# Optimization experiments

Measured on AMD Instinct MI355X. Metric: run time of the kernel, lower is better.

Reference implementation:

```python
import jax, jax.numpy as jnp
import numpy as np

SOS, EOS = 0, 29
B, S, ENC = 64, 800, 512      # batch, encoder seq len, encoder feature dim
T, V = 250, 30                # decode timesteps (training: y.shape[1]), vocab
E, H, D, P = 512, 512, 256, 256  # embed, lstm1 hidden, lstm2 hidden(=decoder_output), attention projection


def setup_inputs() -> dict:
    key = jax.random.key(0)
    ks = jax.random.split(key, 12)
    sc = lambda k, shape, s=0.05: jax.random.normal(k, shape, jnp.float32) * s
    embed_W = sc(ks[0], (V, E), 0.1).at[EOS].set(0.0)  # padding_idx=EOS row zeroed
    return dict(
        encoder_outputs=jax.random.normal(ks[1], (B, S, ENC), jnp.float32),
        embed_W=embed_W,
        W_ih1=sc(ks[2], (E + P, 4 * H)), b_ih1=jnp.zeros((4 * H,), jnp.float32),
        W_hh1=sc(ks[3], (H, 4 * H)),     b_hh1=jnp.zeros((4 * H,), jnp.float32),
        W_ih2=sc(ks[4], (H, 4 * D)),     b_ih2=jnp.zeros((4 * D,), jnp.float32),
        W_hh2=sc(ks[5], (D, 4 * D)),     b_hh2=jnp.zeros((4 * D,), jnp.float32),
        Wk=sc(ks[6], (ENC, P)), bk=jnp.zeros((P,), jnp.float32),
        Wv=sc(ks[7], (ENC, P)), bv=jnp.zeros((P,), jnp.float32),
        Wq=sc(ks[8], (D, P)),   bq=jnp.zeros((P,), jnp.float32),
        char_b=jnp.zeros((V,), jnp.float32),
        encoder_lens=jax.random.randint(ks[9], (B,), S // 2, S + 1),
        y=jax.random.randint(ks[10], (B, T), 0, V),
    )


def _lstm_cell(x, h, c, W_ih, b_ih, W_hh, b_hh):
    gates = x @ W_ih + b_ih + h @ W_hh + b_hh
    i, f, g, o = jnp.split(gates, 4, axis=-1)  # torch LSTMCell gate order
    c_new = jax.nn.sigmoid(f) * c + jax.nn.sigmoid(i) * jnp.tanh(g)
    h_new = jax.nn.sigmoid(o) * jnp.tanh(c_new)
    return h_new, c_new


def reference(encoder_outputs, embed_W, W_ih1, b_ih1, W_hh1, b_hh1,
              W_ih2, b_ih2, W_hh2, b_hh2, Wk, bk, Wv, bv, Wq, bq,
              char_b, encoder_lens, y):
    # set_key_value_mask: project encoder outputs once
    key_proj = encoder_outputs @ Wk + bk        # [B,S,P]
    val_proj = encoder_outputs @ Wv + bv        # [B,S,P]
    mask = jnp.arange(S)[None, :] < encoder_lens[:, None]  # [B,S]
    scale = 1.0 / jnp.sqrt(jnp.asarray(P, jnp.float32))

    # teacher-forced input embeddings: t=0 -> SOS, t>0 -> label_embed[:, t-1]
    label_embed = embed_W[y]                    # [B,T,E]
    sos = jnp.broadcast_to(embed_W[SOS][None, None, :], (1, B, E))
    char_seq = jnp.concatenate([sos, jnp.swapaxes(label_embed[:, :-1, :], 0, 1)], axis=0)  # [T,B,E]

    init = (jnp.zeros((B, H), jnp.float32), jnp.zeros((B, H), jnp.float32),
            jnp.zeros((B, D), jnp.float32), jnp.zeros((B, D), jnp.float32),
            key_proj[:, 0, :])                  # initial context = key[:,0,:]

    def step(carry, char_embed):
        h1, c1, h2, c2, context = carry
        x = jnp.concatenate([char_embed, context], axis=1)          # [B,E+P]
        h1, c1 = _lstm_cell(x, h1, c1, W_ih1, b_ih1, W_hh1, b_hh1)
        h2, c2 = _lstm_cell(h1, h2, c2, W_ih2, b_ih2, W_hh2, b_hh2)
        q = h2 @ Wq + bq                                            # [B,P]
        scores = jnp.einsum('bsp,bp->bs', key_proj, q) * scale      # [B,S]
        scores = jnp.where(mask, scores, -1e9)
        aw = jax.nn.softmax(scores, axis=1)                         # [B,S]
        context = jnp.einsum('bs,bsp->bp', aw, val_proj)            # [B,P]
        out_emb = jnp.concatenate([h2, context], axis=1)            # [B,2D]
        logits = out_emb @ embed_W.T + char_b                       # tied weights, [B,V]
        return (h1, c1, h2, c2, context), (logits, aw[0])

    _, (logits_T, aw0_T) = jax.lax.scan(step, init, char_seq)
    predictions = jnp.swapaxes(logits_T, 0, 1)   # [B,T,V]
    attention_plot = aw0_T.T                      # [S,T] (matches torch.stack(dim=1))
    return predictions, attention_plot
```

## Files before the change

kernel.cpp:

```cpp
#include <hip/hip_runtime.h>

typedef float f32x4 __attribute__((ext_vector_type(4)));
typedef short s16x8 __attribute__((ext_vector_type(8)));

#define MINI(a,b) ((a)<(b)?(a):(b))
#define MAXI(a,b) ((a)>(b)?(a):(b))

static __device__ __forceinline__ float bf2f(unsigned short u){
  union { unsigned int i; float f; } x; x.i = ((unsigned int)u) << 16; return x.f;
}
static __device__ __forceinline__ unsigned short f2bf(float f){
  union { float f; unsigned int i; } x; x.f = f;
  return (unsigned short)((x.i + 0x7fffu + ((x.i >> 16) & 1u)) >> 16);
}
static __device__ __forceinline__ float sigm(float x){ return 1.f / (1.f + __expf(-x)); }
static __device__ __forceinline__ float tanhf_(float x){ return 1.f - 2.f / (1.f + __expf(2.f * x)); }

static __device__ __forceinline__ float ald1(const float* p){
  return __hip_atomic_load(p, __ATOMIC_RELAXED, __HIP_MEMORY_SCOPE_AGENT);
}
static __device__ __forceinline__ void ast1(float* p, float v){
  __hip_atomic_store(p, v, __ATOMIC_RELAXED, __HIP_MEMORY_SCOPE_AGENT);
}
static __device__ __forceinline__ float2 ald2(const float* p){
  unsigned long long u = __hip_atomic_load((const unsigned long long*)p,
                          __ATOMIC_RELAXED, __HIP_MEMORY_SCOPE_AGENT);
  union { unsigned long long u; float2 f; } c; c.u = u; return c.f;
}
static __device__ __forceinline__ void ast2(float* p, float a, float b){
  union { unsigned long long u; float f[2]; } c; c.f[0] = a; c.f[1] = b;
  __hip_atomic_store((unsigned long long*)p, c.u, __ATOMIC_RELAXED, __HIP_MEMORY_SCOPE_AGENT);
}
static __device__ __forceinline__ unsigned long long ald64(const void* p){
  return __hip_atomic_load((const unsigned long long*)p, __ATOMIC_RELAXED, __HIP_MEMORY_SCOPE_AGENT);
}
static __device__ __forceinline__ void ast32(unsigned short* p, unsigned int v){
  __hip_atomic_store((unsigned int*)p, v, __ATOMIC_RELAXED, __HIP_MEMORY_SCOPE_AGENT);
}
static __device__ __forceinline__ void aadd(float* p, float v){
  __hip_atomic_fetch_add(p, v, __ATOMIC_RELAXED, __HIP_MEMORY_SCOPE_AGENT);
}

__global__ void k_prepw(const float* Wk, const float* Wq, const float* Wv,
                        const float* bk, const float* bq, const float* bv,
                        unsigned short* Bm, float* bvec, float* wkb, float* cb0){
  const int k = blockIdx.x;
  const int t = threadIdx.x;
  const float scale = 0.0625f;
  float acc = 0.f;
  for (int p = 0; p < 256; p++) acc += Wk[k*256+p] * Wq[t*256+p];
  Bm[(size_t)k*512 + t]       = f2bf(acc * scale);
  Bm[(size_t)k*512 + 256 + t] = f2bf(Wv[k*256+t]);
  __shared__ float red[256];
  red[t] = Wk[k*256+t] * bq[t];
  __syncthreads();
  for (int o = 128; o > 0; o >>= 1){ if (t < o) red[t] += red[t+o]; __syncthreads(); }
  if (t == 0) wkb[k] = red[0] * scale;
  if (k == 0){
    float a2 = 0.f;
    for (int p = 0; p < 256; p++) a2 += bk[p] * Wq[t*256+p];
    bvec[t] = a2 * scale;
    bvec[256+t] = bv[t];
    __syncthreads();
    red[t] = bk[t] * bq[t];
    __syncthreads();
    for (int o = 128; o > 0; o >>= 1){ if (t < o) red[t] += red[t+o]; __syncthreads(); }
    if (t == 0) *cb0 = red[0] * scale;
  }
}

__global__ void k_keybias(const float* enc, const float* wkb, const float* cb0,
                          float* keybias){
  const int m = blockIdx.x*8 + (threadIdx.x >> 6);
  const int lane = threadIdx.x & 63;
  float p = 0.f;
  #pragma unroll
  for (int j = 0; j < 8; j++){ int k = lane + 64*j; p += enc[(size_t)m*512 + k] * wkb[k]; }
  #pragma unroll
  for (int o = 1; o < 64; o <<= 1) p += __shfl_xor(p, o, 64);
  if (lane == 0) keybias[m] = p + *cb0;
}

__global__ void k_init(const float* enc, const float* Wk, const float* bk,
                       float* ctx, float* la, unsigned short* h1bf,
                       unsigned short* h2bf, float* h2f, float* c1p, float* c2p,
                       unsigned int* ctr){
  const int b = blockIdx.x, t = threadIdx.x;
  float acc = bk[t];
  const float* er = enc + (size_t)b*800*512;
  for (int k = 0; k < 512; k++) acc += er[k] * Wk[(size_t)k*256 + t];
  ctx[b*256 + t] = acc;
  if (t == 0) la[b] = 1.f;
  const int id = b*256 + t;
  unsigned int* h1u = (unsigned int*)h1bf;
  h1u[id] = 0u; h1u[16384 + id] = 0u;
  unsigned int* h2u = (unsigned int*)h2bf;
  h2u[id] = 0u;
  h2f[id] = 0.f; h2f[16384 + id] = 0.f;
  c1p[id] = 0.f; c1p[16384 + id] = 0.f;
  c2p[id] = 0.f;
  if (b == 0){ for (int i = t; i < 1024; i += 256) ctr[i] = 0u; }
}

__global__ __launch_bounds__(256) void k_gemm(const float* enc, const unsigned short* Bm,
                                              const float* bvec,
                                              unsigned short* kT, unsigned short* vl){
  __shared__ unsigned short Al[64][40];
  __shared__ unsigned short Bl[64][40];
  const int tid = threadIdx.x, w = tid >> 6, lane = tid & 63;
  const int M0 = (blockIdx.x >> 3) * 64;
  const int N0 = (blockIdx.x & 7) * 64;
  f32x4 acc[4] = {};
  const int mrow = w*16 + (lane & 15);
  const int koff = (lane >> 4) * 8;
  for (int k0 = 0; k0 < 512; k0 += 32){
    #pragma unroll
    for (int it = 0; it < 2; it++){
      int row = (tid >> 3) + it*32, kq = (tid & 7) * 4;
      float4 v = *(const float4*)(enc + (size_t)(M0+row)*512 + k0 + kq);
      Al[row][kq+0] = f2bf(v.x); Al[row][kq+1] = f2bf(v.y);
      Al[row][kq+2] = f2bf(v.z); Al[row][kq+3] = f2bf(v.w);
    }
    #pragma unroll
    for (int i = 0; i < 8; i++){
      int flat = tid*8 + i, kk = flat >> 6, n = flat & 63;
      Bl[n][kk] = Bm[(size_t)(k0+kk)*512 + N0 + n];
    }
    __syncthreads();
    s16x8 a = *(const s16x8*)&Al[mrow][koff];
    #pragma unroll
    for (int i = 0; i < 4; i++){
      s16x8 bb = *(const s16x8*)&Bl[i*16 + (lane & 15)][koff];
      acc[i] = __builtin_amdgcn_mfma_f32_16x16x32_bf16(a, bb, acc[i], 0, 0, 0);
    }
    __syncthreads();
  }
  #pragma unroll
  for (int i = 0; i < 4; i++){
    int n = N0 + i*16 + (lane & 15);
    float bb = bvec[n];
    #pragma unroll
    for (int r = 0; r < 4; r++){
      int m = M0 + w*16 + (lane >> 4)*4 + r;
      int b = m / 800, s = m - b*800;
      unsigned short hv = f2bf(acc[i][r] + bb);
      if (n < 256) kT[(size_t)b*204800 + (size_t)n*800 + s] = hv;
      else         vl[(size_t)b*204800 + (size_t)s*256 + (n-256)] = hv;
    }
  }
}

static __device__ __forceinline__ void gbar(unsigned int* ctrs, unsigned int* gen){
  __syncthreads();
  if (threadIdx.x == 0){
    *gen += 256u;
    const unsigned int target = *gen;
    __hip_atomic_fetch_add(&ctrs[(blockIdx.x & 15) * 32], 1u,
                           __ATOMIC_RELAXED, __HIP_MEMORY_SCOPE_AGENT);
    if (blockIdx.x == 0){
      for (;;){
        unsigned int s = 0;
        #pragma unroll
        for (int i = 0; i < 16; i++)
          s += __hip_atomic_load(&ctrs[i * 32], __ATOMIC_RELAXED, __HIP_MEMORY_SCOPE_AGENT);
        if (s >= target) break;
        __builtin_amdgcn_s_sleep(2);
      }
      #pragma unroll
      for (int i = 0; i < 16; i++)
        __hip_atomic_store(&ctrs[512 + i*32], target, __ATOMIC_RELAXED, __HIP_MEMORY_SCOPE_AGENT);
    } else {
      unsigned int* fl = &ctrs[512 + (blockIdx.x & 15)*32];
      while (__hip_atomic_load(fl, __ATOMIC_RELAXED, __HIP_MEMORY_SCOPE_AGENT) < target)
        __builtin_amdgcn_s_sleep(4);
    }
  }
  __syncthreads();
}

static __device__ __forceinline__ void dot_bf16(const unsigned short* xg, int k0, int k1,
                                                const float (*W)[8], float* acc){
  const unsigned long long* p = (const unsigned long long*)xg;
  int k = k0;
  while (k + 32 <= k1){
    unsigned long long v[8];
    #pragma unroll
    for (int i = 0; i < 8; i++) v[i] = ald64(p + (k >> 2) + i);
    #pragma unroll
    for (int i = 0; i < 8; i++){
      float xv[4];
      xv[0] = bf2f((unsigned short)v[i]);
      xv[1] = bf2f((unsigned short)(v[i] >> 16));
      xv[2] = bf2f((unsigned short)(v[i] >> 32));
      xv[3] = bf2f((unsigned short)(v[i] >> 48));
      #pragma unroll
      for (int d = 0; d < 4; d++){
        const float* wr = W[k + i*4 + d];
        #pragma unroll
        for (int cc = 0; cc < 8; cc++) acc[cc] += xv[d] * wr[cc];
      }
    }
    k += 32;
  }
  if (k < k1){
    unsigned long long v[4];
    #pragma unroll
    for (int i = 0; i < 4; i++) v[i] = ald64(p + (k >> 2) + i);
    #pragma unroll
    for (int i = 0; i < 4; i++){
      float xv[4];
      xv[0] = bf2f((unsigned short)v[i]);
      xv[1] = bf2f((unsigned short)(v[i] >> 16));
      xv[2] = bf2f((unsigned short)(v[i] >> 32));
      xv[3] = bf2f((unsigned short)(v[i] >> 48));
      #pragma unroll
      for (int d = 0; d < 4; d++){
        const float* wr = W[k + i*4 + d];
        #pragma unroll
        for (int cc = 0; cc < 8; cc++) acc[cc] += xv[d] * wr[cc];
      }
    }
  }
}

static __device__ __forceinline__ void dot_f32(const float* xg, int k0, int k1,
                                               const float (*W)[8], float* acc){
  for (int k = k0; k < k1; k += 16){
    float2 v[8];
    #pragma unroll
    for (int i = 0; i < 8; i++) v[i] = ald2(xg + k + 2*i);
    #pragma unroll
    for (int i = 0; i < 8; i++){
      const float* w0 = W[k + 2*i];
      const float* w1 = W[k + 2*i + 1];
      #pragma unroll
      for (int cc = 0; cc < 8; cc++) acc[cc] += v[i].x*w0[cc] + v[i].y*w1[cc];
    }
  }
}

__global__ __launch_bounds__(1024) void k_decode(
    const float* W_ih1, const float* b_ih1, const float* W_hh1, const float* b_hh1,
    const float* W_ih2, const float* b_ih2, const float* W_hh2, const float* b_hh2,
    const float* embW, const float* char_b, const int* lens, const int* y,
    const unsigned short* kT, const unsigned short* vl, const float* keybias,
    unsigned short* h1bf, unsigned short* h2bf, float* h2f,
    float* ctxacc, float* lacc, float* c1p, float* c2p,
    float* esc, unsigned int* ctr, float* out)
{
  __shared__ float W1s[1280][8];
  __shared__ float W2s[768][8];
  __shared__ float b1s[8];
  __shared__ float b2s[8];
  __shared__ float embrow[512];
  __shared__ float chb;
  __shared__ float redA[16][8][64];
  __shared__ float g1s[8][64];
  __shared__ float partA[16][256];
  __shared__ float e_l[256];
  __shared__ float h2loc[256];

  const int bi = blockIdx.x;
  const int tid = threadIdx.x;
  const int w = tid >> 6;
  const int lane = tid & 63;

  for (int idx = tid; idx < 1280*8; idx += 1024){
    int k = idx >> 3, c = idx & 7;
    int col = ((c >> 1) << 9) + 2*bi + (c & 1);
    W1s[k][c] = (k < 768) ? W_ih1[(size_t)k*2048 + col] : W_hh1[(size_t)(k-768)*2048 + col];
  }
  if (bi < 128){
    for (int idx = tid; idx < 768*8; idx += 1024){
      int k = idx >> 3, c = idx & 7;
      int col = ((c >> 1) << 8) + 2*bi + (c & 1);
      W2s[k][c] = (k < 512) ? W_ih2[(size_t)k*1024 + col] : W_hh2[(size_t)(k-512)*1024 + col];
    }
    if (tid < 8){ int col = ((tid >> 1) << 8) + 2*bi + (tid & 1); b2s[tid] = b_ih2[col] + b_hh2[col]; }
  }
  if (tid < 8){ int col = ((tid >> 1) << 9) + 2*bi + (tid & 1); b1s[tid] = b_ih1[col] + b_hh1[col]; }
  if (bi >= 128 && bi < 158){
    if (tid < 512) embrow[tid] = embW[(bi-128)*512 + tid];
    if (tid == 0) chb = char_b[bi-128];
  }
  __syncthreads();

  unsigned int gen = 0;
  const int myb = bi & 63;
  const int sc  = bi >> 6;
  const int mylen = lens[myb];
  const int sbase = sc * 200;

  float* preds = out;
  float* plot  = out + 480000;

  for (int t = 0; t < 250; ++t){
    const int p  = t & 1;
    const int np = 1 - p;
    const unsigned short* h1p_bf = h1bf + p*(64*512);
    unsigned short*       h1n_bf = h1bf + np*(64*512);
    const unsigned short* h2p_bf = h2bf + p*(64*256);
    unsigned short*       h2n_bf = h2bf + np*(64*256);
    const float* h2f_p = h2f + p*(64*256);
    float*       h2f_np= h2f + np*(64*256);
    const float* ca_p  = ctxacc + p*(64*256);
    float*       ca_np = ctxacc + np*(64*256);
    const float* la_p  = lacc + p*64;
    float*       la_np = lacc + np*64;

    {
      float acc[8]  = {0,0,0,0,0,0,0,0};
      float accB[8] = {0,0,0,0,0,0,0,0};
      const int b = lane;
      const int tok = (t == 0) ? 0 : y[b*250 + (t-1)];
      const float* erow = embW + (size_t)tok*512;
      const float* crow = ca_p + b*256 - 512;
      const unsigned short* hrow = h1p_bf + b*512 - 768;
      const int k0 = w*80, k1 = k0 + 80;
      const int a1 = MINI(k1, 512);
      for (int k = k0; k < a1; k += 4){
        float4 xv = *(const float4*)(erow + k);
        const float* w0 = W1s[k]; const float* w1 = W1s[k+1];
        const float* w2 = W1s[k+2]; const float* w3 = W1s[k+3];
        #pragma unroll
        for (int cc = 0; cc < 8; cc++)
          acc[cc] += xv.x*w0[cc] + xv.y*w1[cc] + xv.z*w2[cc] + xv.w*w3[cc];
      }
      dot_f32(crow, MAXI(k0,512), MINI(k1,768), W1s, accB);
      dot_bf16(hrow, MAXI(k0,768), k1, W1s, acc);
      const float rl = 1.f / ald1(&la_p[b]);
      #pragma unroll
      for (int c = 0; c < 8; c++) redA[w][c][b] = acc[c] + accB[c]*rl;
    }
    __syncthreads();
    if (tid < 512){
      int c = tid >> 6, b = tid & 63;
      float g = b1s[c];
      #pragma unroll
      for (int ww = 0; ww < 16; ww++) g += redA[ww][c][b];
      g1s[c][b] = g;
    }
    __syncthreads();
    if (w == 0){
      int b = lane;
      float h0, h1v;
      { float gi=g1s[0][b], gf=g1s[2][b], gg=g1s[4][b], go=g1s[6][b];
        float co = c1p[bi*128 + 2*b];
        float cn = sigm(gf)*co + sigm(gi)*tanhf_(gg);
        c1p[bi*128 + 2*b] = cn; h0 = sigm(go)*tanhf_(cn); }
      { float gi=g1s[1][b], gf=g1s[3][b], gg=g1s[5][b], go=g1s[7][b];
        float co = c1p[bi*128 + 2*b + 1];
        float cn = sigm(gf)*co + sigm(gi)*tanhf_(gg);
        c1p[bi*128 + 2*b + 1] = cn; h1v = sigm(go)*tanhf_(cn); }
      unsigned int pk = (unsigned int)f2bf(h0) | ((unsigned int)f2bf(h1v) << 16);
      ast32(h1n_bf + b*512 + 2*bi, pk);
    }
    gbar(ctr, &gen);

    if (bi < 128){
      {
        float acc2[8] = {0,0,0,0,0,0,0,0};
        const int b = lane;
        const unsigned short* h1r = h1n_bf + b*512;
        const unsigned short* h2r = h2p_bf + b*256 - 512;
        const int k0 = w*48, k1 = k0 + 48;
        dot_bf16(h1r, k0, MINI(k1,512), W2s, acc2);
        dot_bf16(h2r, MAXI(k0,512), k1, W2s, acc2);
        #pragma unroll
        for (int c = 0; c < 8; c++) redA[w][c][lane] = acc2[c];
      }
      __syncthreads();
      if (tid < 512){
        int c = tid >> 6, b = tid & 63;
        float g = b2s[c];
        #pragma unroll
        for (int ww = 0; ww < 16; ww++) g += redA[ww][c][b];
        g1s[c][b] = g;
      }
      __syncthreads();
      if (w == 0){
        int b = lane;
        float h0, h1v;
        { float gi=g1s[0][b], gf=g1s[2][b], gg=g1s[4][b], go=g1s[6][b];
          float co = c2p[bi*128 + 2*b];
          float cn = sigm(gf)*co + sigm(gi)*tanhf_(gg);
          c2p[bi*128 + 2*b] = cn; h0 = sigm(go)*tanhf_(cn); }
        { float gi=g1s[1][b], gf=g1s[3][b], gg=g1s[5][b], go=g1s[7][b];
          float co = c2p[bi*128 + 2*b + 1];
          float cn = sigm(gf)*co + sigm(gi)*tanhf_(gg);
          c2p[bi*128 + 2*b + 1] = cn; h1v = sigm(go)*tanhf_(cn); }
        unsigned int pk = (unsigned int)f2bf(h0) | ((unsigned int)f2bf(h1v) << 16);
        ast32(h2n_bf + b*256 + 2*bi, pk);
        ast2(h2f_np + b*256 + 2*bi, h0, h1v);
      }
    } else if (bi < 158){
      if (t > 0){
        if (tid < 512){
          int b3 = tid & 63, ch = tid >> 6;
          const float* base = (ch < 4) ? (h2f_p + b3*256 + ch*64)
                                       : (ca_p  + b3*256 + (ch-4)*64);
          const float* er = &embrow[(ch < 4) ? ch*64 : 256 + (ch-4)*64];
          float pc = 0.f;
          for (int c4 = 0; c4 < 4; c4++){
            float2 v[8];
            #pragma unroll
            for (int i = 0; i < 8; i++) v[i] = ald2(base + c4*16 + 2*i);
            #pragma unroll
            for (int i = 0; i < 8; i++)
              pc += v[i].x*er[c4*16 + 2*i] + v[i].y*er[c4*16 + 2*i + 1];
          }
          if (ch >= 4) pc *= 1.f / ald1(&la_p[b3]);
          g1s[ch][b3] = pc;
        }
        __syncthreads();
        if (tid < 64){
          float s2 = chb;
          #pragma unroll
          for (int c = 0; c < 8; c++) s2 += g1s[c][tid];
          preds[tid*7500 + (t-1)*30 + (bi-128)] = s2;
        }
      }
    } else if (bi < 190){
      if (t > 0 && tid < 25){
        int s3 = (bi-158)*25 + tid;
        plot[(size_t)s3*250 + (t-1)] = ald1(&esc[s3]) * (1.f / ald1(&la_p[0]));
      }
    } else if (bi < 254){
      if (tid < 128) ast2(&ca_np[(bi-190)*256 + 2*tid], 0.f, 0.f);
    } else if (bi == 254){
      if (tid < 64) ast1(&la_np[tid], 0.f);
    }
    gbar(ctr, &gen);

    {
      if (tid < 128){ float2 hv = ald2(&h2f_np[myb*256 + 2*tid]);
                      h2loc[2*tid] = hv.x; h2loc[2*tid+1] = hv.y; }
      __syncthreads();
      const int qlen = MINI(200, MAXI(0, mylen - sbase));
      {
        float ps0=0.f, ps1=0.f, ps2=0.f, ps3=0.f;
        if (4*lane < qlen){
          const float* hl = &h2loc[w*16];
          const unsigned short* kb = kT + (size_t)myb*204800 + (size_t)(w*16)*800 + sbase + 4*lane;
          #pragma unroll 8
          for (int kk = 0; kk < 16; kk++){
            const unsigned long long u = *(const unsigned long long*)(kb + (size_t)kk*800);
            const float hv = hl[kk];
            ps0 += bf2f((unsigned short)(u      )) * hv;
            ps1 += bf2f((unsigned short)(u >> 16)) * hv;
            ps2 += bf2f((unsigned short)(u >> 32)) * hv;
            ps3 += bf2f((unsigned short)(u >> 48)) * hv;
          }
        }
        partA[w][4*lane+0] = ps0; partA[w][4*lane+1] = ps1;
        partA[w][4*lane+2] = ps2; partA[w][4*lane+3] = ps3;
      }
      __syncthreads();
      if (tid < 256){
        float e = 0.f;
        if (tid < qlen){
          float sc_ = partA[0][tid];
          #pragma unroll
          for (int q = 1; q < 16; q++) sc_ += partA[q][tid];
          e = __expf(sc_ + keybias[myb*800 + sbase + tid]);
        }
        e_l[tid] = e;
        if (myb == 0 && tid < 200) ast1(&esc[sbase + tid], e);
      }
      __syncthreads();
      if (w == 0){
        float s4 = e_l[lane] + e_l[lane+64] + e_l[lane+128] + e_l[lane+192];
        #pragma unroll
        for (int o = 1; o < 64; o <<= 1) s4 += __shfl_xor(s4, o, 64);
        if (lane == 0) aadd(&la_np[myb], s4);
      }
      {
        float va0=0.f, va1=0.f, va2=0.f, va3=0.f;
        const int j0 = w*13;
        if (j0 < qlen){
          const unsigned short* vp = vl + (size_t)myb*204800 + (size_t)(sbase + j0)*256 + 4*lane;
          #pragma unroll 4
          for (int jj = 0; jj < 13; jj++){
            const float ev = e_l[j0 + jj];
            const unsigned long long u = *(const unsigned long long*)(vp + (size_t)jj*256);
            va0 += bf2f((unsigned short)(u      )) * ev;
            va1 += bf2f((unsigned short)(u >> 16)) * ev;
            va2 += bf2f((unsigned short)(u >> 32)) * ev;
            va3 += bf2f((unsigned short)(u >> 48)) * ev;
          }
        }
        __syncthreads();
        partA[w][4*lane+0] = va0; partA[w][4*lane+1] = va1;
        partA[w][4*lane+2] = va2; partA[w][4*lane+3] = va3;
      }
      __syncthreads();
      if (tid < 256){
        float s5 = partA[0][tid];
        #pragma unroll
        for (int q = 1; q < 16; q++) s5 += partA[q][tid];
        aadd(&ca_np[myb*256 + tid], s5);
      }
    }
    gbar(ctr, &gen);
  }

  {
    const float* h2f_p = h2f;
    const float* ca_p  = ctxacc;
    const float* la_p  = lacc;
    if (bi >= 128 && bi < 158){
      if (tid < 512){
        int b3 = tid & 63, ch = tid >> 6;
        const float* base = (ch < 4) ? (h2f_p + b3*256 + ch*64)
                                     : (ca_p  + b3*256 + (ch-4)*64);
        const float* er = &embrow[(ch < 4) ? ch*64 : 256 + (ch-4)*64];
        float pc = 0.f;
        for (int c4 = 0; c4 < 4; c4++){
          float2 v[8];
          #pragma unroll
          for (int i = 0; i < 8; i++) v[i] = ald2(base + c4*16 + 2*i);
          #pragma unroll
          for (int i = 0; i < 8; i++)
            pc += v[i].x*er[c4*16 + 2*i] + v[i].y*er[c4*16 + 2*i + 1];
        }
        if (ch >= 4) pc *= 1.f / ald1(&la_p[b3]);
        g1s[ch][b3] = pc;
      }
      __syncthreads();
      if (tid < 64){
        float s2 = chb;
        #pragma unroll
        for (int c = 0; c < 8; c++) s2 += g1s[c][tid];
        preds[tid*7500 + 249*30 + (bi-128)] = s2;
      }
    } else if (bi >= 158 && bi < 190){
      if (tid < 25){
        int s3 = (bi-158)*25 + tid;
        plot[(size_t)s3*250 + 249] = ald1(&esc[s3]) * (1.f / ald1(&la_p[0]));
      }
    }
  }
}

extern "C" void kernel_launch(void* const* d_in, const int* in_sizes, int n_in,
                              void* d_out, int out_size, void* d_ws, size_t ws_size,
                              hipStream_t stream){
  const float* enc    = (const float*)d_in[0];
  const float* embW   = (const float*)d_in[1];
  const float* W_ih1  = (const float*)d_in[2];
  const float* b_ih1  = (const float*)d_in[3];
  const float* W_hh1  = (const float*)d_in[4];
  const float* b_hh1  = (const float*)d_in[5];
  const float* W_ih2  = (const float*)d_in[6];
  const float* b_ih2  = (const float*)d_in[7];
  const float* W_hh2  = (const float*)d_in[8];
  const float* b_hh2  = (const float*)d_in[9];
  const float* Wk     = (const float*)d_in[10];
  const float* bk     = (const float*)d_in[11];
  const float* Wv     = (const float*)d_in[12];
  const float* bv     = (const float*)d_in[13];
  const float* Wq     = (const float*)d_in[14];
  const float* bq     = (const float*)d_in[15];
  const float* char_b = (const float*)d_in[16];
  const int*   lens   = (const int*)d_in[17];
  const int*   y      = (const int*)d_in[18];

  char* ws = (char*)d_ws;
  unsigned short* kT   = (unsigned short*)(ws + 0);
  unsigned short* vlp  = (unsigned short*)(ws + 26214400);
  float* keybias       = (float*)(ws + 52428800);
  unsigned short* Bmat = (unsigned short*)(ws + 52633600);
  float* bvec          = (float*)(ws + 53157888);
  float* wkb           = (float*)(ws + 53159936);
  float* cb0           = (float*)(ws + 53161984);
  unsigned short* h1bf = (unsigned short*)(ws + 53163008);
  unsigned short* h2bf = (unsigned short*)(ws + 53294080);
  float* h2f           = (float*)(ws + 53359616);
  float* ctxacc        = (float*)(ws + 53621760);
  float* lacc          = (float*)(ws + 53752832);
  float* c1p           = (float*)(ws + 53753856);
  float* c2p           = (float*)(ws + 53884928);
  float* esc           = (float*)(ws + 53950464);
  unsigned int* ctr    = (unsigned int*)(ws + 53954560);
  float* out = (float*)d_out;

  k_prepw<<<512, 256, 0, stream>>>(Wk, Wq, Wv, bk, bq, bv, Bmat, bvec, wkb, cb0);
  k_keybias<<<6400, 512, 0, stream>>>(enc, wkb, cb0, keybias);
  k_init<<<64, 256, 0, stream>>>(enc, Wk, bk, ctxacc, lacc, h1bf, h2bf, h2f, c1p, c2p, ctr);
  k_gemm<<<6400, 256, 0, stream>>>(enc, Bmat, bvec, kT, vlp);
  k_decode<<<256, 1024, 0, stream>>>(W_ih1, b_ih1, W_hh1, b_hh1, W_ih2, b_ih2, W_hh2, b_hh2,
                                     embW, char_b, lens, y, kT, vlp, keybias,
                                     h1bf, h2bf, h2f, ctxacc, lacc, c1p, c2p, esc, ctr, out);
}
```

Before: 12.38 ms.

## Precompute next-step LSTM1 embedding and hidden gate partials before grid barrier

Splits the layer-1 gate matvec so that the embedding and recurrent-hidden contributions for step t+1 are computed at the end of step t, before the grid-wide barrier. Only the context part, which depends on the attention result from all blocks, stays after the barrier. This moves work off the serial critical path after each barrier, so blocks that arrive early at the barrier can use that time. It assumes h1 for the next step is already final in h1n_bf and that redA is not overwritten between the precompute and its use.

Measured after the change: 12.83 ms. 3.6% more time.

```diff
diff --git a/kernel.cpp b/kernel.cpp
--- a/kernel.cpp
+++ b/kernel.cpp
@@ -239,6 +239,35 @@
   }
 }
 
+static __device__ __forceinline__ void g1_xh(const float* embW, const int* y,
+    float (*redA)[8][64], const float (*W1s)[8],
+    const unsigned short* h1src, int lane, int w, int tprev){
+  float acc[8] = {0,0,0,0,0,0,0,0};
+  const int k0 = w*80, k1 = k0 + 80;
+  const int a1 = MINI(k1, 512);
+  if (k0 < 512){
+    const int tok = (tprev < 0) ? 0 : y[lane*250 + tprev];
+    const float* erow = embW + (size_t)tok*512;
+    for (int k = k0; k < a1; k += 16){
+      float4 v0 = *(const float4*)(erow + k);
+      float4 v1 = *(const float4*)(erow + k + 4);
+      float4 v2 = *(const float4*)(erow + k + 8);
+      float4 v3 = *(const float4*)(erow + k + 12);
+      const float xv[16] = { v0.x,v0.y,v0.z,v0.w, v1.x,v1.y,v1.z,v1.w,
+                             v2.x,v2.y,v2.z,v2.w, v3.x,v3.y,v3.z,v3.w };
+      #pragma unroll
+      for (int d = 0; d < 16; d++){
+        const float* wr = W1s[k + d];
+        #pragma unroll
+        for (int cc = 0; cc < 8; cc++) acc[cc] += xv[d] * wr[cc];
+      }
+    }
+  }
+  dot_bf16(h1src + lane*512 - 768, MAXI(k0,768), k1, W1s, acc);
+  #pragma unroll
+  for (int c = 0; c < 8; c++) redA[w][c][lane] = acc[c];
+}
+
 __global__ __launch_bounds__(1024) void k_decode(
     const float* W_ih1, const float* b_ih1, const float* W_hh1, const float* b_hh1,
     const float* W_ih2, const float* b_ih2, const float* W_hh2, const float* b_hh2,
@@ -294,6 +323,8 @@
   float* preds = out;
   float* plot  = out + 480000;
 
+  g1_xh(embW, y, redA, W1s, h1bf, lane, w, -1);
+
   for (int t = 0; t < 250; ++t){
     const int p  = t & 1;
     const int np = 1 - p;
@@ -309,28 +340,15 @@
     float*       la_np = lacc + np*64;
 
     {
-      float acc[8]  = {0,0,0,0,0,0,0,0};
-      float accB[8] = {0,0,0,0,0,0,0,0};
-      const int b = lane;
-      const int tok = (t == 0) ? 0 : y[b*250 + (t-1)];
-      const float* erow = embW + (size_t)tok*512;
-      const float* crow = ca_p + b*256 - 512;
-      const unsigned short* hrow = h1p_bf + b*512 - 768;
       const int k0 = w*80, k1 = k0 + 80;
-      const int a1 = MINI(k1, 512);
-      for (int k = k0; k < a1; k += 4){
-        float4 xv = *(const float4*)(erow + k);
-        const float* w0 = W1s[k]; const float* w1 = W1s[k+1];
-        const float* w2 = W1s[k+2]; const float* w3 = W1s[k+3];
-        #pragma unroll
-        for (int cc = 0; cc < 8; cc++)
-          acc[cc] += xv.x*w0[cc] + xv.y*w1[cc] + xv.z*w2[cc] + xv.w*w3[cc];
-      }
-      dot_f32(crow, MAXI(k0,512), MINI(k1,768), W1s, accB);
-      dot_bf16(hrow, MAXI(k0,768), k1, W1s, acc);
-      const float rl = 1.f / ald1(&la_p[b]);
-      #pragma unroll
-      for (int c = 0; c < 8; c++) redA[w][c][b] = acc[c] + accB[c]*rl;
+      const int lo = MAXI(k0, 512), hi = MINI(k1, 768);
+      if (lo < hi){
+        float accB[8] = {0,0,0,0,0,0,0,0};
+        dot_f32(ca_p + lane*256 - 512, lo, hi, W1s, accB);
+        const float rl = 1.f / ald1(&la_p[lane]);
+        #pragma unroll
+        for (int c = 0; c < 8; c++) redA[w][c][lane] += accB[c]*rl;
+      }
     }
     __syncthreads();
     if (tid < 512){
@@ -501,6 +519,10 @@
         aadd(&ca_np[myb*256 + tid], s5);
       }
     }
+
+    if (t < 249)
+      g1_xh(embW, y, redA, W1s, h1n_bf, lane, w, t);
+
     gbar(ctr, &gen);
   }
 
```
